# Performance work log

Hardware: AMD Instinct MI355X
Metric: run time of the kernel (lower is better)

Reference implementation:

```python
import jax, jax.numpy as jnp
import numpy as np
from jax import lax

DECAY = 0.99
EPS = 1e-5


def setup_inputs() -> dict:
    key = jax.random.key(0)
    k1, k2, k3 = jax.random.split(key, 3)
    x = jax.random.normal(k1, (32, 64, 64, 64), dtype=jnp.float32)  # NCHW, C == embedding_dim
    embedding = jax.random.normal(k2, (512, 64), dtype=jnp.float32)  # [K, D] codebook
    cluster_size = jnp.ones((512,), dtype=jnp.float32)  # EMA buffer
    embedding_avg = jax.random.normal(k3, (512, 64), dtype=jnp.float32)  # EMA buffer
    return {"x": x, "embedding": embedding, "cluster_size": cluster_size, "embedding_avg": embedding_avg}


def reference(x, embedding, cluster_size, embedding_avg):
    n, c, h, w = x.shape
    K, D = embedding.shape
    # [N, D] flattened tokens (NHWC order, matching permute(0,2,3,1))
    flat_x = jnp.transpose(x, (0, 2, 3, 1)).reshape(-1, D)
    distances = (
        jnp.sum(flat_x ** 2, axis=1, keepdims=True)
        + jnp.sum(embedding ** 2, axis=1)
        - 2.0 * flat_x @ embedding.T
    )  # [N, K]
    idxs = jnp.argmin(distances, axis=1)  # [N]
    # one_hot @ embedding == gather (same math, no [N,K] one-hot GEMM)
    quantized = embedding[idxs].reshape(n, h, w, c)
    quantized = jnp.transpose(quantized, (0, 3, 1, 2))  # back to NCHW
    loss = jnp.mean((x - lax.stop_gradient(quantized)) ** 2)
    # EMA updates (training path). segment_sum == one_hot.sum(0) / flat_x.T @ one_hot
    ones = jnp.ones((flat_x.shape[0],), dtype=x.dtype)
    batch_cluster_size = jax.ops.segment_sum(ones, idxs, num_segments=K)  # [K]
    batch_embedding_avg = jax.ops.segment_sum(flat_x, idxs, num_segments=K)  # [K, D]
    new_cluster_size = cluster_size * DECAY + (1.0 - DECAY) * batch_cluster_size
    new_embedding_avg = embedding_avg * DECAY + (1.0 - DECAY) * batch_embedding_avg
    new_embedding = new_embedding_avg / (new_cluster_size + EPS)[:, None]
    # straight-through estimator
    quantized_st = x + lax.stop_gradient(quantized - x)
    return quantized_st, loss, new_embedding, new_cluster_size, new_embedding_avg
```

## Files before the change

### kernel.cpp

```cpp
#include <hip/hip_runtime.h>

#define HW 4096
#define KC 512

typedef __attribute__((ext_vector_type(8))) short s16x8;
typedef __attribute__((ext_vector_type(16))) float f32x16;

__device__ inline short f2bf(float f) {
    unsigned int u = __builtin_bit_cast(unsigned int, f);
    unsigned int lsb = (u >> 16) & 1u;
    u += 0x7fffu + lsb;
    return (short)(u >> 16);
}
__device__ inline float bf2f(short h) {
    unsigned int u = ((unsigned int)(unsigned short)h) << 16;
    return __builtin_bit_cast(float, u);
}

#define WS_EN    133136
#define WS_EHF   135184
#define WS_ELF   217104
#define WS_CAND  282640

__global__ void k_prep_en(const float* __restrict__ emb, float* __restrict__ en) {
    int m = blockIdx.x * 256 + threadIdx.x;
    if (m >= KC) return;
    const float* e = emb + m * 64;
    float d0 = 0.f, d1 = 0.f, d2 = 0.f, d3 = 0.f;
#pragma unroll
    for (int c = 0; c < 64; c += 4) {
        d0 = fmaf(e[c], e[c], d0);
        d1 = fmaf(e[c + 1], e[c + 1], d1);
        d2 = fmaf(e[c + 2], e[c + 2], d2);
        d3 = fmaf(e[c + 3], e[c + 3], d3);
    }
    en[m] = (d0 + d1) + (d2 + d3);
}

__global__ void k_prep_frag(const float* __restrict__ emb, const float* __restrict__ en,
                            short* __restrict__ ehf, short* __restrict__ elf) {
    int t = blockIdx.x * 256 + threadIdx.x;
    int m = t >> 3, ko = t & 7;
    int mt = m >> 5, ks = ko >> 1;
    int lane = (m & 31) + 32 * (ko & 1);
    s16x8 hv, lv;
#pragma unroll
    for (int j = 0; j < 8; ++j) {
        float v = emb[m * 64 + ko * 8 + j];
        short h = f2bf(v);
        hv[j] = h;
        lv[j] = f2bf(v - bf2f(h));
    }
    ((s16x8*)ehf)[(mt * 5 + ks) * 64 + lane] = hv;
    ((s16x8*)elf)[(mt * 4 + ks) * 64 + lane] = lv;

    int e2 = t * 2;
    int mt2 = e2 >> 9;
    int lane2 = (e2 >> 3) & 63;
    int j2 = e2 & 7;
    unsigned int val = 0;
    if (lane2 < 32 && j2 == 0) {
        float ev = en[mt2 * 32 + (lane2 & 31)];
        short eh_ = f2bf(ev);
        short el_ = f2bf(ev - bf2f(eh_));
        val = ((unsigned int)(unsigned short)eh_) | (((unsigned int)(unsigned short)el_) << 16);
    }
    *(unsigned int*)(ehf + ((size_t)(mt2 * 5 + 4) * 64 + lane2) * 8 + j2) = val;
}

__device__ inline void merge2(float& s1, int& i1, float& s2, int& i2,
                              float os1, int oi1, float os2, int oi2) {
    bool ob = (os1 < s1) || (os1 == s1 && oi1 < i1);
    float n1s = ob ? os1 : s1;  int n1i = ob ? oi1 : i1;
    float ls  = ob ? s1  : os1; int li  = ob ? i1  : oi1;
    float ws  = ob ? os2 : s2;  int wi  = ob ? oi2 : i2;
    bool b2 = (ls < ws) || (ls == ws && li < wi);
    s1 = n1s; i1 = n1i;
    s2 = b2 ? ls : ws; i2 = b2 ? li : wi;
}

__global__ __launch_bounds__(256) void k_argmin(const float* __restrict__ x,
                                                const short* __restrict__ ehf,
                                                const short* __restrict__ elf,
                                                unsigned int* __restrict__ cand) {
    int tid = threadIdx.x;
    int wv = tid >> 6, lane = tid & 63;
    int tb = blockIdx.x * 128;
    int n = tb >> 12, hwb = tb & 4095;
    const float* xp = x + (size_t)n * 64 * HW;
    int wbase = hwb + wv * 32;

    int l5 = lane & 31;
    int kh = (lane >> 5) * 8;

    s16x8 fh[5], fl[4];
    {
        const float* pa = xp + wbase + l5;
#pragma unroll
        for (int ks = 0; ks < 4; ++ks) {
            s16x8 ha, la;
#pragma unroll
            for (int j = 0; j < 8; ++j) {
                int c = ks * 16 + kh + j;
                float va = -2.0f * pa[(size_t)c * HW];
                short h0 = f2bf(va); ha[j] = h0; la[j] = f2bf(va - bf2f(h0));
            }
            fh[ks] = ha; fl[ks] = la;
        }
        s16x8 v0;
#pragma unroll
        for (int j = 0; j < 8; ++j) v0[j] = 0;
        if (lane < 32) { v0[0] = (short)0x3F80; v0[1] = (short)0x3F80; }
        fh[4] = v0;
    }

    const s16x8* eh8 = (const s16x8*)ehf;
    const s16x8* el8 = (const s16x8*)elf;

    float s1 = 3.402823466e38f, s2 = 3.402823466e38f;
    int i1 = 0, i2 = 0;
    int hv4 = (lane >> 5) * 4;

#pragma unroll 2
    for (int mt = 0; mt < 16; ++mt) {
        s16x8 ah[5], al[4];
#pragma unroll
        for (int ks = 0; ks < 5; ++ks) ah[ks] = eh8[(mt * 5 + ks) * 64 + lane];
#pragma unroll
        for (int ks = 0; ks < 4; ++ks) al[ks] = el8[(mt * 4 + ks) * 64 + lane];

        f32x16 acc;
#pragma unroll
        for (int r = 0; r < 16; ++r) acc[r] = 0.0f;
#pragma unroll
        for (int ks = 0; ks < 5; ++ks)
            acc = __builtin_amdgcn_mfma_f32_32x32x16_bf16(ah[ks], fh[ks], acc, 0, 0, 0);
#pragma unroll
        for (int ks = 0; ks < 4; ++ks)
            acc = __builtin_amdgcn_mfma_f32_32x32x16_bf16(al[ks], fh[ks], acc, 0, 0, 0);
#pragma unroll
        for (int ks = 0; ks < 4; ++ks)
            acc = __builtin_amdgcn_mfma_f32_32x32x16_bf16(ah[ks], fl[ks], acc, 0, 0, 0);

        int mb = mt * 32 + hv4;
#pragma unroll
        for (int r = 0; r < 16; ++r) {
            int mi = mb + (r & 3) + 8 * (r >> 2);
            float s = acc[r];
            bool c1 = s < s1, c2 = s < s2;
            s2 = c1 ? s1 : (c2 ? s : s2); i2 = c1 ? i1 : (c2 ? mi : i2);
            s1 = c1 ? s : s1;             i1 = c1 ? mi : i1;
        }
    }

    merge2(s1, i1, s2, i2, __shfl_xor(s1, 32), __shfl_xor(i1, 32),
           __shfl_xor(s2, 32), __shfl_xor(i2, 32));

    if (lane < 32)
        cand[tb + wv * 32 + l5] = (unsigned int)i1 | ((unsigned int)i2 << 16);
}

__global__ __launch_bounds__(256) void k_quant(const float* __restrict__ x,
                                               const float* __restrict__ emb,
                                               const float* __restrict__ en,
                                               unsigned int* __restrict__ cand,
                                               float* __restrict__ qout,
                                               float* __restrict__ loss_acc) {
    int t = blockIdx.x * 256 + threadIdx.x;
    int n = t >> 12, hw = t & 4095;
    const float* xq = x + (size_t)n * 64 * HW + hw;

    float xv[64];
#pragma unroll
    for (int c = 0; c < 64; ++c) xv[c] = xq[(size_t)c * HW];

    unsigned int cd = cand[t];
    int c1 = (int)(cd & 0xffffu), c2 = (int)(cd >> 16);
    int ia = (c1 < c2) ? c1 : c2;
    int ib = (c1 < c2) ? c2 : c1;

    float sxx;
    {
        float d0 = 0.f, d1 = 0.f, d2 = 0.f, d3 = 0.f;
#pragma unroll
        for (int c = 0; c < 64; c += 4) {
            d0 = fmaf(xv[c], xv[c], d0);
            d1 = fmaf(xv[c + 1], xv[c + 1], d1);
            d2 = fmaf(xv[c + 2], xv[c + 2], d2);
            d3 = fmaf(xv[c + 3], xv[c + 3], d3);
        }
        sxx = (d0 + d1) + (d2 + d3);
    }

    float sa, sb;
    {
        const float4* er = (const float4*)(emb + (size_t)ia * 64);
        float d0 = 0.f, d1 = 0.f, d2 = 0.f, d3 = 0.f;
#pragma unroll
        for (int q = 0; q < 16; ++q) {
            float4 e4 = er[q];
            d0 = fmaf(xv[q * 4], e4.x, d0);
            d1 = fmaf(xv[q * 4 + 1], e4.y, d1);
            d2 = fmaf(xv[q * 4 + 2], e4.z, d2);
            d3 = fmaf(xv[q * 4 + 3], e4.w, d3);
        }
        sa = (sxx + en[ia]) - 2.0f * ((d0 + d1) + (d2 + d3));
    }
    {
        const float4* er = (const float4*)(emb + (size_t)ib * 64);
        float d0 = 0.f, d1 = 0.f, d2 = 0.f, d3 = 0.f;
#pragma unroll
        for (int q = 0; q < 16; ++q) {
            float4 e4 = er[q];
            d0 = fmaf(xv[q * 4], e4.x, d0);
            d1 = fmaf(xv[q * 4 + 1], e4.y, d1);
            d2 = fmaf(xv[q * 4 + 2], e4.z, d2);
            d3 = fmaf(xv[q * 4 + 3], e4.w, d3);
        }
        sb = (sxx + en[ib]) - 2.0f * ((d0 + d1) + (d2 + d3));
    }
    int win = (sb < sa) ? ib : ia;
    cand[t] = (unsigned int)win;

    const float4* ew = (const float4*)(emb + (size_t)win * 64);
    float* qp = qout + (size_t)n * 64 * HW + hw;
    float l0 = 0.f, l1 = 0.f, l2 = 0.f, l3 = 0.f;
#pragma unroll
    for (int q = 0; q < 16; ++q) {
        float4 e4 = ew[q];
        qp[(size_t)(q * 4) * HW] = e4.x;
        qp[(size_t)(q * 4 + 1) * HW] = e4.y;
        qp[(size_t)(q * 4 + 2) * HW] = e4.z;
        qp[(size_t)(q * 4 + 3) * HW] = e4.w;
        float f0 = xv[q * 4] - e4.x, f1 = xv[q * 4 + 1] - e4.y;
        float f2 = xv[q * 4 + 2] - e4.z, f3 = xv[q * 4 + 3] - e4.w;
        l0 = fmaf(f0, f0, l0);
        l1 = fmaf(f1, f1, l1);
        l2 = fmaf(f2, f2, l2);
        l3 = fmaf(f3, f3, l3);
    }
    float lp = (l0 + l1) + (l2 + l3);
#pragma unroll
    for (int off = 32; off; off >>= 1) lp += __shfl_down(lp, off);
    if ((threadIdx.x & 63) == 0) atomicAdd(loss_acc, lp);
}

__global__ __launch_bounds__(1024) void k_seg(const float* __restrict__ x,
                                              const unsigned int* __restrict__ idx,
                                              float* __restrict__ cnt_g,
                                              float* __restrict__ avg_g) {
    __shared__ float acc[KC * 9];
    __shared__ float cnt[KC];
    int tid = threadIdx.x;
    int b = blockIdx.x;
    int n = b >> 4;
    int cg = (b >> 1) & 7;
    int h = b & 1;

    for (int i = tid; i < KC * 9; i += 1024) acc[i] = 0.f;
    if (cg == 0 && tid < KC) cnt[tid] = 0.f;
    __syncthreads();

    const float* xp = x + (size_t)n * 64 * HW + (size_t)(cg * 8) * HW + h * 2048;
    const unsigned int* ip = idx + n * HW + h * 2048;

#pragma unroll
    for (int p = 0; p < 2; ++p) {
        int hw = p * 1024 + tid;
        int k = (int)ip[hw];
        if (cg == 0) atomicAdd(&cnt[k], 1.0f);
        float* row = acc + k * 9;
#pragma unroll
        for (int j = 0; j < 8; ++j) {
            atomicAdd(&row[j], xp[(size_t)j * HW + hw]);
        }
    }
    __syncthreads();

    for (int i = tid; i < KC * 8; i += 1024) {
        int k = i >> 3, j = i & 7;
        atomicAdd(&avg_g[k * 64 + cg * 8 + j], acc[k * 9 + j]);
    }
    if (cg == 0 && tid < KC) atomicAdd(&cnt_g[tid], cnt[tid]);
}

__global__ void k_fin(const float* __restrict__ cs_in, const float* __restrict__ avg_in,
                      const float* __restrict__ cnt, const float* __restrict__ avgacc,
                      const float* __restrict__ loss_acc,
                      float* __restrict__ loss_out, float* __restrict__ emb_out,
                      float* __restrict__ cs_out, float* __restrict__ avg_out) {
    int i = blockIdx.x * 256 + threadIdx.x;
    if (i >= KC * 64) return;
    int k = i >> 6, c = i & 63;
    float ncs = cs_in[k] * 0.99f + 0.01f * cnt[k];
    float nav = avg_in[i] * 0.99f + 0.01f * avgacc[i];
    avg_out[i] = nav;
    emb_out[i] = nav / (ncs + 1e-5f);
    if (c == 0) cs_out[k] = ncs;
    if (i == 0) loss_out[0] = loss_acc[0] * (1.0f / 8388608.0f);
}

extern "C" void kernel_launch(void* const* d_in, const int* in_sizes, int n_in,
                              void* d_out, int out_size, void* d_ws, size_t ws_size,
                              hipStream_t stream) {
    (void)in_sizes; (void)n_in; (void)out_size; (void)ws_size;
    const float* x   = (const float*)d_in[0];
    const float* emb = (const float*)d_in[1];
    const float* cs  = (const float*)d_in[2];
    const float* avg = (const float*)d_in[3];

    float* out      = (float*)d_out;
    float* qout     = out;
    float* loss_out = out + 8388608;
    float* emb_out  = loss_out + 1;
    float* cs_out   = emb_out + 32768;
    float* avg_out  = cs_out + 512;

    char* wsb = (char*)d_ws;
    float* cnt_acc  = (float*)wsb;
    float* avg_acc  = (float*)(wsb + 2048);
    float* loss_acc = (float*)(wsb + 133120);
    float* en       = (float*)(wsb + WS_EN);
    short* ehf      = (short*)(wsb + WS_EHF);
    short* elf      = (short*)(wsb + WS_ELF);
    unsigned int* cand = (unsigned int*)(wsb + WS_CAND);

    hipMemsetAsync(d_ws, 0, 133124, stream);
    k_prep_en<<<2, 256, 0, stream>>>(emb, en);
    k_prep_frag<<<16, 256, 0, stream>>>(emb, en, ehf, elf);
    k_argmin<<<1024, 256, 0, stream>>>(x, ehf, elf, cand);
    k_quant<<<512, 256, 0, stream>>>(x, emb, en, cand, qout, loss_acc);
    k_seg<<<512, 1024, 0, stream>>>(x, cand, cnt_acc, avg_acc);
    k_fin<<<128, 256, 0, stream>>>(cs, avg, cnt_acc, avg_acc, loss_acc,
                                   loss_out, emb_out, cs_out, avg_out);
}
```

Before: 168.8 us.

## Fuse segment-sum into quantize kernel with per-block partials reduced in finalize

Removes the separate segment-sum kernel. The quantize kernel now runs 1024-thread blocks and, once it has the winning index, accumulates counts and full 64-channel sums into a padded shared-memory table using the x values already held in registers, so x is not read a second time. Each block writes its table as a partial record to workspace, and the finalize kernel sums the 128 partials per element; if workspace is too small it falls back to global atomics. In exchange it uses about 133KB of shared memory per block, which may limit occupancy or not fit, adds 64 shared atomics per thread with possible contention on popular codes, and adds a 17MB partial buffer that finalize must read.

```diff
diff --git a/kernel.cpp b/kernel.cpp
--- a/kernel.cpp
+++ b/kernel.cpp
@@ -21,6 +21,9 @@
 #define WS_EHF   135184
 #define WS_ELF   217104
 #define WS_CAND  282640
+#define WS_PART  806928
+#define NPART    128
+#define PART_REC 33280
 
 __global__ void k_prep_en(const float* __restrict__ emb, float* __restrict__ en) {
     int m = blockIdx.x * 256 + threadIdx.x;
@@ -160,13 +163,24 @@
         cand[tb + wv * 32 + l5] = (unsigned int)i1 | ((unsigned int)i2 << 16);
 }
 
-__global__ __launch_bounds__(256) void k_quant(const float* __restrict__ x,
-                                               const float* __restrict__ emb,
-                                               const float* __restrict__ en,
-                                               unsigned int* __restrict__ cand,
-                                               float* __restrict__ qout,
-                                               float* __restrict__ loss_acc) {
-    int t = blockIdx.x * 256 + threadIdx.x;
+__global__ __launch_bounds__(1024) void k_quant(const float* __restrict__ x,
+                                                const float* __restrict__ emb,
+                                                const float* __restrict__ en,
+                                                const unsigned int* __restrict__ cand,
+                                                float* __restrict__ qout,
+                                                float* __restrict__ loss_acc,
+                                                float* __restrict__ cnt_g,
+                                                float* __restrict__ avg_g,
+                                                float* __restrict__ part,
+                                                int nparts) {
+    __shared__ float acc[KC * 65];
+    __shared__ float cnt[KC];
+
+    int tid = threadIdx.x;
+    for (int i = tid; i < KC * 65; i += 1024) acc[i] = 0.f;
+    if (tid < KC) cnt[tid] = 0.f;
+
+    int t = blockIdx.x * 1024 + tid;
     int n = t >> 12, hw = t & 4095;
     const float* xq = x + (size_t)n * 64 * HW + hw;
 
@@ -220,7 +234,6 @@
         sb = (sxx + en[ib]) - 2.0f * ((d0 + d1) + (d2 + d3));
     }
     int win = (sb < sa) ? ib : ia;
-    cand[t] = (unsigned int)win;
 
     const float4* ew = (const float4*)(emb + (size_t)win * 64);
     float* qp = qout + (size_t)n * 64 * HW + hw;
@@ -242,58 +255,53 @@
     float lp = (l0 + l1) + (l2 + l3);
 #pragma unroll
     for (int off = 32; off; off >>= 1) lp += __shfl_down(lp, off);
-    if ((threadIdx.x & 63) == 0) atomicAdd(loss_acc, lp);
-}
-
-__global__ __launch_bounds__(1024) void k_seg(const float* __restrict__ x,
-                                              const unsigned int* __restrict__ idx,
-                                              float* __restrict__ cnt_g,
-                                              float* __restrict__ avg_g) {
-    __shared__ float acc[KC * 9];
-    __shared__ float cnt[KC];
-    int tid = threadIdx.x;
-    int b = blockIdx.x;
-    int n = b >> 4;
-    int cg = (b >> 1) & 7;
-    int h = b & 1;
-
-    for (int i = tid; i < KC * 9; i += 1024) acc[i] = 0.f;
-    if (cg == 0 && tid < KC) cnt[tid] = 0.f;
+    if ((tid & 63) == 0) atomicAdd(loss_acc, lp);
+
     __syncthreads();
 
-    const float* xp = x + (size_t)n * 64 * HW + (size_t)(cg * 8) * HW + h * 2048;
-    const unsigned int* ip = idx + n * HW + h * 2048;
-
-#pragma unroll
-    for (int p = 0; p < 2; ++p) {
-        int hw = p * 1024 + tid;
-        int k = (int)ip[hw];
-        if (cg == 0) atomicAdd(&cnt[k], 1.0f);
-        float* row = acc + k * 9;
-#pragma unroll
-        for (int j = 0; j < 8; ++j) {
-            atomicAdd(&row[j], xp[(size_t)j * HW + hw]);
-        }
-    }
+    atomicAdd(&cnt[win], 1.0f);
+    float* row = acc + win * 65;
+#pragma unroll
+    for (int c = 0; c < 64; ++c) atomicAdd(&row[c], xv[c]);
+
     __syncthreads();
 
-    for (int i = tid; i < KC * 8; i += 1024) {
-        int k = i >> 3, j = i & 7;
-        atomicAdd(&avg_g[k * 64 + cg * 8 + j], acc[k * 9 + j]);
-    }
-    if (cg == 0 && tid < KC) atomicAdd(&cnt_g[tid], cnt[tid]);
+    if (nparts) {
+        float* pr = part + (size_t)blockIdx.x * PART_REC;
+        for (int i = tid; i < KC * 65; i += 1024) pr[i] = acc[i];
+    } else {
+        for (int i = tid; i < KC * 64; i += 1024)
+            atomicAdd(&avg_g[i], acc[(i >> 6) * 65 + (i & 63)]);
+    }
+    if (tid < KC) atomicAdd(&cnt_g[tid], cnt[tid]);
 }
 
 __global__ void k_fin(const float* __restrict__ cs_in, const float* __restrict__ avg_in,
                       const float* __restrict__ cnt, const float* __restrict__ avgacc,
+                      const float* __restrict__ part, int nparts,
                       const float* __restrict__ loss_acc,
                       float* __restrict__ loss_out, float* __restrict__ emb_out,
                       float* __restrict__ cs_out, float* __restrict__ avg_out) {
     int i = blockIdx.x * 256 + threadIdx.x;
     if (i >= KC * 64) return;
     int k = i >> 6, c = i & 63;
+    float bsum;
+    if (nparts) {
+        float a0 = 0.f, a1 = 0.f, a2 = 0.f, a3 = 0.f;
+        size_t off = (size_t)k * 65 + c;
+#pragma unroll 4
+        for (int b = 0; b < NPART; b += 4) {
+            a0 += part[(size_t)b * PART_REC + off];
+            a1 += part[(size_t)(b + 1) * PART_REC + off];
+            a2 += part[(size_t)(b + 2) * PART_REC + off];
+            a3 += part[(size_t)(b + 3) * PART_REC + off];
+        }
+        bsum = (a0 + a1) + (a2 + a3);
+    } else {
+        bsum = avgacc[i];
+    }
     float ncs = cs_in[k] * 0.99f + 0.01f * cnt[k];
-    float nav = avg_in[i] * 0.99f + 0.01f * avgacc[i];
+    float nav = avg_in[i] * 0.99f + 0.01f * bsum;
     avg_out[i] = nav;
     emb_out[i] = nav / (ncs + 1e-5f);
     if (c == 0) cs_out[k] = ncs;
@@ -303,7 +311,7 @@
 extern "C" void kernel_launch(void* const* d_in, const int* in_sizes, int n_in,
                               void* d_out, int out_size, void* d_ws, size_t ws_size,
                               hipStream_t stream) {
-    (void)in_sizes; (void)n_in; (void)out_size; (void)ws_size;
+    (void)in_sizes; (void)n_in; (void)out_size;
     const float* x   = (const float*)d_in[0];
     const float* emb = (const float*)d_in[1];
     const float* cs  = (const float*)d_in[2];
@@ -324,13 +332,16 @@
     short* ehf      = (short*)(wsb + WS_EHF);
     short* elf      = (short*)(wsb + WS_ELF);
     unsigned int* cand = (unsigned int*)(wsb + WS_CAND);
+    float* part     = (float*)(wsb + WS_PART);
+
+    int nparts = (ws_size >= (size_t)WS_PART + (size_t)NPART * PART_REC * 4) ? NPART : 0;
 
     hipMemsetAsync(d_ws, 0, 133124, stream);
     k_prep_en<<<2, 256, 0, stream>>>(emb, en);
     k_prep_frag<<<16, 256, 0, stream>>>(emb, en, ehf, elf);
     k_argmin<<<1024, 256, 0, stream>>>(x, ehf, elf, cand);
-    k_quant<<<512, 256, 0, stream>>>(x, emb, en, cand, qout, loss_acc);
-    k_seg<<<512, 1024, 0, stream>>>(x, cand, cnt_acc, avg_acc);
-    k_fin<<<128, 256, 0, stream>>>(cs, avg, cnt_acc, avg_acc, loss_acc,
+    k_quant<<<128, 1024, 0, stream>>>(x, emb, en, cand, qout, loss_acc,
+                                      cnt_acc, avg_acc, part, nparts);
+    k_fin<<<128, 256, 0, stream>>>(cs, avg, cnt_acc, avg_acc, part, nparts, loss_acc,
                                    loss_out, emb_out, cs_out, avg_out);
 }
```

Measured after the change: 254.9 us. 51.0% more time.

## Replace global atomics in segment-sum with per-block partials reduced in finalize

Applied to the files above, without the earlier changes.

k_seg now runs one block per (image, channel group) over all 4096 pixels instead of half, which halves the block count and the number of global flushes. When the workspace is large enough, each block writes its shared-memory partial sums to a dedicated workspace record instead of issuing global atomicAdds, and k_fin sums the 32 partials per element. The x loads are also hoisted ahead of the LDS atomics to overlap memory latency. In exchange it adds about 4 MB of partial writes and reads, and the finalize kernel does more work.

```diff
diff --git a/kernel.cpp b/kernel.cpp
--- a/kernel.cpp
+++ b/kernel.cpp
@@ -21,6 +21,8 @@
 #define WS_EHF   135184
 #define WS_ELF   217104
 #define WS_CAND  282640
+#define WS_PART  806928
+#define PART_REC 4096
 
 __global__ void k_prep_en(const float* __restrict__ emb, float* __restrict__ en) {
     int m = blockIdx.x * 256 + threadIdx.x;
@@ -248,52 +250,85 @@
 __global__ __launch_bounds__(1024) void k_seg(const float* __restrict__ x,
                                               const unsigned int* __restrict__ idx,
                                               float* __restrict__ cnt_g,
-                                              float* __restrict__ avg_g) {
+                                              float* __restrict__ avg_g,
+                                              float* __restrict__ part,
+                                              int nparts) {
     __shared__ float acc[KC * 9];
     __shared__ float cnt[KC];
     int tid = threadIdx.x;
-    int b = blockIdx.x;
-    int n = b >> 4;
-    int cg = (b >> 1) & 7;
-    int h = b & 1;
+    int n = blockIdx.x >> 3;
+    int cg = blockIdx.x & 7;
 
     for (int i = tid; i < KC * 9; i += 1024) acc[i] = 0.f;
     if (cg == 0 && tid < KC) cnt[tid] = 0.f;
     __syncthreads();
 
-    const float* xp = x + (size_t)n * 64 * HW + (size_t)(cg * 8) * HW + h * 2048;
-    const unsigned int* ip = idx + n * HW + h * 2048;
-
-#pragma unroll
-    for (int p = 0; p < 2; ++p) {
+    const float* xp = x + (size_t)n * 64 * HW + (size_t)(cg * 8) * HW;
+    const unsigned int* ip = idx + n * HW;
+
+#pragma unroll
+    for (int p = 0; p < 4; ++p) {
         int hw = p * 1024 + tid;
         int k = (int)ip[hw];
+        float v0 = xp[hw];
+        float v1 = xp[(size_t)1 * HW + hw];
+        float v2 = xp[(size_t)2 * HW + hw];
+        float v3 = xp[(size_t)3 * HW + hw];
+        float v4 = xp[(size_t)4 * HW + hw];
+        float v5 = xp[(size_t)5 * HW + hw];
+        float v6 = xp[(size_t)6 * HW + hw];
+        float v7 = xp[(size_t)7 * HW + hw];
         if (cg == 0) atomicAdd(&cnt[k], 1.0f);
         float* row = acc + k * 9;
-#pragma unroll
-        for (int j = 0; j < 8; ++j) {
-            atomicAdd(&row[j], xp[(size_t)j * HW + hw]);
-        }
+        atomicAdd(&row[0], v0);
+        atomicAdd(&row[1], v1);
+        atomicAdd(&row[2], v2);
+        atomicAdd(&row[3], v3);
+        atomicAdd(&row[4], v4);
+        atomicAdd(&row[5], v5);
+        atomicAdd(&row[6], v6);
+        atomicAdd(&row[7], v7);
     }
     __syncthreads();
 
-    for (int i = tid; i < KC * 8; i += 1024) {
-        int k = i >> 3, j = i & 7;
-        atomicAdd(&avg_g[k * 64 + cg * 8 + j], acc[k * 9 + j]);
+    if (nparts) {
+        float* pr = part + (size_t)blockIdx.x * PART_REC;
+        for (int i = tid; i < KC * 8; i += 1024)
+            pr[i] = acc[(i >> 3) * 9 + (i & 7)];
+    } else {
+        for (int i = tid; i < KC * 8; i += 1024)
+            atomicAdd(&avg_g[(i >> 3) * 64 + cg * 8 + (i & 7)], acc[(i >> 3) * 9 + (i & 7)]);
     }
     if (cg == 0 && tid < KC) atomicAdd(&cnt_g[tid], cnt[tid]);
 }
 
 __global__ void k_fin(const float* __restrict__ cs_in, const float* __restrict__ avg_in,
                       const float* __restrict__ cnt, const float* __restrict__ avgacc,
+                      const float* __restrict__ part, int nparts,
                       const float* __restrict__ loss_acc,
                       float* __restrict__ loss_out, float* __restrict__ emb_out,
                       float* __restrict__ cs_out, float* __restrict__ avg_out) {
     int i = blockIdx.x * 256 + threadIdx.x;
     if (i >= KC * 64) return;
     int k = i >> 6, c = i & 63;
+    float bsum;
+    if (nparts) {
+        int cg = c >> 3, j = c & 7;
+        size_t off = (size_t)(k * 8 + j);
+        float a0 = 0.f, a1 = 0.f, a2 = 0.f, a3 = 0.f;
+#pragma unroll
+        for (int n = 0; n < 32; n += 4) {
+            a0 += part[(size_t)((n + 0) * 8 + cg) * PART_REC + off];
+            a1 += part[(size_t)((n + 1) * 8 + cg) * PART_REC + off];
+            a2 += part[(size_t)((n + 2) * 8 + cg) * PART_REC + off];
+            a3 += part[(size_t)((n + 3) * 8 + cg) * PART_REC + off];
+        }
+        bsum = (a0 + a1) + (a2 + a3);
+    } else {
+        bsum = avgacc[i];
+    }
     float ncs = cs_in[k] * 0.99f + 0.01f * cnt[k];
-    float nav = avg_in[i] * 0.99f + 0.01f * avgacc[i];
+    float nav = avg_in[i] * 0.99f + 0.01f * bsum;
     avg_out[i] = nav;
     emb_out[i] = nav / (ncs + 1e-5f);
     if (c == 0) cs_out[k] = ncs;
@@ -303,7 +338,7 @@
 extern "C" void kernel_launch(void* const* d_in, const int* in_sizes, int n_in,
                               void* d_out, int out_size, void* d_ws, size_t ws_size,
                               hipStream_t stream) {
-    (void)in_sizes; (void)n_in; (void)out_size; (void)ws_size;
+    (void)in_sizes; (void)n_in; (void)out_size;
     const float* x   = (const float*)d_in[0];
     const float* emb = (const float*)d_in[1];
     const float* cs  = (const float*)d_in[2];
@@ -324,13 +359,16 @@
     short* ehf      = (short*)(wsb + WS_EHF);
     short* elf      = (short*)(wsb + WS_ELF);
     unsigned int* cand = (unsigned int*)(wsb + WS_CAND);
+    float* part     = (float*)(wsb + WS_PART);
+
+    int nparts = (ws_size >= (size_t)WS_PART + (size_t)256 * PART_REC * 4) ? 1 : 0;
 
     hipMemsetAsync(d_ws, 0, 133124, stream);
     k_prep_en<<<2, 256, 0, stream>>>(emb, en);
     k_prep_frag<<<16, 256, 0, stream>>>(emb, en, ehf, elf);
     k_argmin<<<1024, 256, 0, stream>>>(x, ehf, elf, cand);
     k_quant<<<512, 256, 0, stream>>>(x, emb, en, cand, qout, loss_acc);
-    k_seg<<<512, 1024, 0, stream>>>(x, cand, cnt_acc, avg_acc);
-    k_fin<<<128, 256, 0, stream>>>(cs, avg, cnt_acc, avg_acc, loss_acc,
+    k_seg<<<256, 1024, 0, stream>>>(x, cand, cnt_acc, avg_acc, part, nparts);
+    k_fin<<<128, 256, 0, stream>>>(cs, avg, cnt_acc, avg_acc, part, nparts, loss_acc,
                                    loss_out, emb_out, cs_out, avg_out);
 }
```

New measurement: 169.2 us (median of 2 runs). No clear change (+0.3%).
